# Kernel optimization log

Hardware: AMD Instinct MI355X
Metric: run time of the kernel (lower is better)

Reference implementation:

```python
import jax, jax.numpy as jnp
import numpy as np

N_WIN = 7
NUM_HEADS = 8
DIM = 256
QK = 256
TOPK = 4
MLP_HID = 4 * DIM
SCALE = QK ** -0.5  # used for both region routing and pixel attention (qk_scale=None)


def _layernorm(x, g, b, eps=1e-6):
    mu = jnp.mean(x, axis=-1, keepdims=True)
    var = jnp.mean(jnp.square(x - mu), axis=-1, keepdims=True)
    return (x - mu) * jax.lax.rsqrt(var + eps) * g + b


def _dwconv(x, w, b):
    # x: NHWC, w: (5,5,1,C) depthwise kernel (torch Conv2d groups=C, padding=2)
    y = jax.lax.conv_general_dilated(
        x, w, window_strides=(1, 1), padding='SAME',
        feature_group_count=x.shape[-1],
        dimension_numbers=('NHWC', 'HWIO', 'NHWC'))
    return y + b


def _bra(x, qkv_w, qkv_b, lepe_w, lepe_b, wo_w, wo_b):
    # BiLevelRoutingAttention, NHWC in/out
    N, H, W, C = x.shape
    j = i = N_WIN
    h, w = H // j, W // i
    p2, w2, m = j * i, h * w, NUM_HEADS
    dq, dv = QK // m, C // m
    # window partition: (N, p2, h, w, C)
    xw = x.reshape(N, j, h, i, w, C).transpose(0, 1, 3, 2, 4, 5).reshape(N, p2, h, w, C)
    qkv = xw @ qkv_w + qkv_b
    q = qkv[..., :QK]            # (N,p2,h,w,QK)
    kv = qkv[..., QK:]           # (N,p2,h,w,QK+C)
    q_pix = q.reshape(N, p2, w2, QK)
    kv_pix = kv.reshape(N, p2, w2, QK + C)
    q_win = jnp.mean(q, axis=(2, 3))                    # (N,p2,QK)
    k_win = jnp.mean(kv[..., :QK], axis=(2, 3))         # (N,p2,QK)
    # LePE: depthwise conv on V in full-image layout
    v_img = kv[..., QK:].reshape(N, j, i, h, w, C).transpose(0, 1, 3, 2, 4, 5).reshape(N, H, W, C)
    lepe = _dwconv(v_img, lepe_w, lepe_b)
    # region-to-region routing, top-k window selection
    logit = jnp.einsum('npc,nqc->npq', q_win * SCALE, k_win)    # (N,p2,p2)
    _, r_idx = jax.lax.top_k(logit, TOPK)                       # (N,p2,TOPK)
    # gather KV of selected windows: (N,p2,TOPK,w2,QK+C)
    kv_sel = kv_pix[jnp.arange(N)[:, None, None], r_idx]
    k_sel = kv_sel[..., :QK].reshape(N, p2, TOPK * w2, m, dq).transpose(0, 1, 3, 2, 4)  # (N,p2,m,kw2,dq)
    v_sel = kv_sel[..., QK:].reshape(N, p2, TOPK * w2, m, dv).transpose(0, 1, 3, 2, 4)  # (N,p2,m,kw2,dv)
    q_h = q_pix.reshape(N, p2, w2, m, dq).transpose(0, 1, 3, 2, 4)                      # (N,p2,m,w2,dq)
    aw = jnp.einsum('npmqd,npmkd->npmqk', q_h * SCALE, k_sel)
    aw = jax.nn.softmax(aw, axis=-1)
    out = jnp.einsum('npmqk,npmkd->npmqd', aw, v_sel)           # (N,p2,m,w2,dv)
    out = out.transpose(0, 1, 3, 2, 4).reshape(N, j, i, h, w, C)
    out = out.transpose(0, 1, 3, 2, 4, 5).reshape(N, H, W, C)
    out = out + lepe
    return out @ wo_w + wo_b


def setup_inputs() -> dict:
    key = jax.random.key(0)
    ks = jax.random.split(key, 8)
    s = 0.02
    return {
        'x': jax.random.normal(ks[0], (8, 56, 56, DIM), dtype=jnp.float32),
        'ln1_g': jnp.ones((DIM,), jnp.float32),
        'ln1_b': jnp.zeros((DIM,), jnp.float32),
        'qkv_w': jax.random.normal(ks[1], (DIM, 2 * QK + DIM), jnp.float32) * s,
        'qkv_b': jnp.zeros((2 * QK + DIM,), jnp.float32),
        'lepe_w': jax.random.normal(ks[2], (5, 5, 1, DIM), jnp.float32) * s,
        'lepe_b': jnp.zeros((DIM,), jnp.float32),
        'wo_w': jax.random.normal(ks[3], (DIM, DIM), jnp.float32) * s,
        'wo_b': jnp.zeros((DIM,), jnp.float32),
        'ln2_g': jnp.ones((DIM,), jnp.float32),
        'ln2_b': jnp.zeros((DIM,), jnp.float32),
        'mlp_w1': jax.random.normal(ks[4], (DIM, MLP_HID), jnp.float32) * s,
        'mlp_b1': jnp.zeros((MLP_HID,), jnp.float32),
        'mlp_w2': jax.random.normal(ks[5], (MLP_HID, DIM), jnp.float32) * s,
        'mlp_b2': jnp.zeros((DIM,), jnp.float32),
    }


def reference(x, ln1_g, ln1_b, qkv_w, qkv_b, lepe_w, lepe_b, wo_w, wo_b,
              ln2_g, ln2_b, mlp_w1, mlp_b1, mlp_w2, mlp_b2):
    x = x + _bra(_layernorm(x, ln1_g, ln1_b), qkv_w, qkv_b, lepe_w, lepe_b, wo_w, wo_b)
    h = _layernorm(x, ln2_g, ln2_b)
    h = jax.nn.gelu(h @ mlp_w1 + mlp_b1, approximate=False) @ mlp_w2 + mlp_b2
    return x + h
```

## Files before the change

### kernel.cpp

```cpp
#include <hip/hip_runtime.h>
#include <hip/hip_bf16.h>

#define NIMG 8
#define HW 56
#define CDIM 256
#define TOK (NIMG*HW*HW)
#define NWIN 49
#define NPW (NIMG*NWIN)
#define ATT_SCALE 0.0625f

typedef __attribute__((ext_vector_type(8))) short short8;
typedef __attribute__((ext_vector_type(4))) short short4v;
typedef __attribute__((ext_vector_type(4))) float f32x4;

static const size_t OFF_WQKV  = 0;
static const size_t OFF_WWO   = 393216;
static const size_t OFF_W1    = 524288;
static const size_t OFF_W2    = 1048576;
static const size_t OFF_XLN   = 1572864;
static const size_t OFF_QKV   = 14417920;
static const size_t OFF_QKWIN = 52953088;
static const size_t OFF_RIDX  = 53755904;
static const size_t OFF_ATTN  = 53762176;
static const size_t OFF_HMID  = OFF_XLN;

__device__ __forceinline__ float gelu_exact(float v) {
    return 0.5f * v * (1.f + erff(v * 0.70710678118654752f));
}
__device__ __forceinline__ short f2bs(float x) {
    __hip_bfloat16 h = __float2bfloat16(x);
    return *(short*)&h;
}
__device__ __forceinline__ float bs2f(short s) {
    return __uint_as_float(((unsigned)(unsigned short)s) << 16);
}
__device__ __forceinline__ void gld16(const short* g, short* l) {
    __builtin_amdgcn_global_load_lds(
        (const __attribute__((address_space(1))) void*)g,
        (__attribute__((address_space(3))) void*)l, 16, 0, 0);
}

__global__ __launch_bounds__(256) void transpose_cast4_k(const float* __restrict__ s0,
                                                         const float* __restrict__ s1,
                                                         const float* __restrict__ s2,
                                                         const float* __restrict__ s3,
                                                         __hip_bfloat16* __restrict__ d0,
                                                         __hip_bfloat16* __restrict__ d1,
                                                         __hip_bfloat16* __restrict__ d2,
                                                         __hip_bfloat16* __restrict__ d3) {
    int b = blockIdx.x;
    const float* src; __hip_bfloat16* dst; int K, N, l;
    if (b < 192)      { src = s0; dst = d0; K = 256;  N = 768;  l = b; }
    else if (b < 256) { src = s1; dst = d1; K = 256;  N = 256;  l = b - 192; }
    else if (b < 512) { src = s2; dst = d2; K = 256;  N = 1024; l = b - 256; }
    else              { src = s3; dst = d3; K = 1024; N = 256;  l = b - 512; }
    int nx = N / 32;
    int n0 = (l % nx) * 32, k0 = (l / nx) * 32;
    __shared__ float t[32][33];
    int tx = threadIdx.x & 31, ty = threadIdx.x >> 5;
    #pragma unroll
    for (int i = 0; i < 32; i += 8)
        t[ty + i][tx] = src[(size_t)(k0 + ty + i) * N + n0 + tx];
    __syncthreads();
    #pragma unroll
    for (int i = 0; i < 32; i += 8)
        dst[(size_t)(n0 + ty + i) * K + k0 + tx] = __float2bfloat16(t[tx][ty + i]);
}

__global__ __launch_bounds__(256) void ln_bf_k(const float* __restrict__ in,
                                               const float* __restrict__ g,
                                               const float* __restrict__ b,
                                               short* __restrict__ out, int remap) {
    int t = blockIdx.x * 4 + (threadIdx.x >> 6);
    int lane = threadIdx.x & 63;
    float4 v = *(const float4*)(in + (size_t)t * 256 + lane * 4);
    float s = v.x + v.y + v.z + v.w;
    float s2 = v.x * v.x + v.y * v.y + v.z * v.z + v.w * v.w;
    #pragma unroll
    for (int o = 32; o > 0; o >>= 1) {
        s  += __shfl_xor(s, o);
        s2 += __shfl_xor(s2, o);
    }
    float mu = s * (1.f / 256.f);
    float rstd = rsqrtf(s2 * (1.f / 256.f) - mu * mu + 1e-6f);
    float4 gv = *(const float4*)(g + lane * 4);
    float4 bv = *(const float4*)(b + lane * 4);
    short4v o;
    o[0] = f2bs((v.x - mu) * rstd * gv.x + bv.x);
    o[1] = f2bs((v.y - mu) * rstd * gv.y + bv.y);
    o[2] = f2bs((v.z - mu) * rstd * gv.z + bv.z);
    o[3] = f2bs((v.w - mu) * rstd * gv.w + bv.w);
    size_t tb;
    if (remap) {
        int n = t / 3136, rem = t % 3136, y = rem / 56, x = rem % 56;
        int p = (y >> 3) * 7 + (x >> 3);
        int si = (y & 7) * 8 + (x & 7);
        tb = (size_t)(n * 49 + p) * 64 + si;
    } else {
        tb = (size_t)t;
    }
    *(short4v*)(out + tb * 256 + lane * 4) = o;
}

__device__ __forceinline__ void mfma_step(const short* As, const short* Bs,
                                          int wm, int wn, int l15, int swr,
                                          f32x4 acc[2][4]) {
    short8 af[2], bfr[4];
    #pragma unroll
    for (int i = 0; i < 2; ++i)
        af[i] = *(const short8*)&As[(wm + i * 16 + l15) * 32 + swr];
    #pragma unroll
    for (int j = 0; j < 4; ++j)
        bfr[j] = *(const short8*)&Bs[(wn + j * 16 + l15) * 32 + swr];
    #pragma unroll
    for (int i = 0; i < 2; ++i)
        #pragma unroll
        for (int j = 0; j < 4; ++j)
            acc[i][j] = __builtin_amdgcn_mfma_f32_16x16x32_bf16(af[i], bfr[j], acc[i][j], 0, 0, 0);
}

template<int MODE>
__global__ __launch_bounds__(256) void gemm64(const short* __restrict__ A,
                                              const short* __restrict__ Bt,
                                              const float* __restrict__ bias,
                                              const float* __restrict__ res,
                                              void* Cv, float* __restrict__ winptr,
                                              int M, int N, int K) {
    const int bn = blockIdx.x * 128;
    const int bm = blockIdx.y * 64;
    const int tid = threadIdx.x;
    const int wave = tid >> 6, lane = tid & 63;
    const int l15 = lane & 15, quad = lane >> 4;
    const int wm = (wave & 1) * 32, wn = (wave >> 1) * 64;

    __shared__ __align__(16) short smem[18432];

    f32x4 acc[2][4];
    #pragma unroll
    for (int i = 0; i < 2; ++i)
        #pragma unroll
        for (int j = 0; j < 4; ++j) acc[i][j] = (f32x4){0.f, 0.f, 0.f, 0.f};

    const int srow = lane >> 2;
    const int scg  = ((lane & 3) ^ ((lane >> 3) & 3)) * 8;
    const short* ga  = A  + (size_t)(bm + wave * 16 + srow) * K + scg;
    const short* gb0 = Bt + (size_t)(bn + wave * 16 + srow) * K + scg;
    const short* gb1 = gb0 + (size_t)64 * K;
    const int swr = (quad ^ ((l15 >> 1) & 3)) * 8;

    const int nt = K >> 5;

    {
        short* b0 = smem;
        gld16(ga,       b0 + wave * 512);
        gld16(gb0,      b0 + 2048 + wave * 512);
        gld16(gb1,      b0 + 4096 + wave * 512);
        short* b1 = smem + 6144;
        gld16(ga  + 32, b1 + wave * 512);
        gld16(gb0 + 32, b1 + 2048 + wave * 512);
        gld16(gb1 + 32, b1 + 4096 + wave * 512);
    }

    for (int t = 0; t < nt; ++t) {
        if (t == nt - 1) asm volatile("s_waitcnt vmcnt(0)" ::: "memory");
        else             asm volatile("s_waitcnt vmcnt(3)" ::: "memory");
        __builtin_amdgcn_s_barrier();
        asm volatile("" ::: "memory");
        if (t + 2 < nt) {
            short* b = smem + ((t + 2) % 3) * 6144;
            int kk = (t + 2) * 32;
            gld16(ga  + kk, b + wave * 512);
            gld16(gb0 + kk, b + 2048 + wave * 512);
            gld16(gb1 + kk, b + 4096 + wave * 512);
        }
        const short* As = smem + (t % 3) * 6144;
        mfma_step(As, As + 2048, wm, wn, l15, swr, acc);
    }

    if (MODE == 0) {
        if (bn < 512) {
            float* wmean = (float*)&smem[12288];
            #pragma unroll
            for (int j = 0; j < 4; ++j) {
                float s = 0.f;
                #pragma unroll
                for (int i = 0; i < 2; ++i)
                    #pragma unroll
                    for (int r = 0; r < 4; ++r) s += acc[i][j][r];
                s += __shfl_xor(s, 16);
                s += __shfl_xor(s, 32);
                if (quad == 0) wmean[wave * 64 + j * 16 + l15] = s;
            }
            __syncthreads();
            if (tid < 128) {
                int c = tid;
                float s = (c < 64) ? (wmean[c] + wmean[64 + c])
                                   : (wmean[64 + c] + wmean[128 + c]);
                int col = bn + c;
                if (col < 512)
                    winptr[(size_t)blockIdx.y * 512 + col] = s * (1.f / 64.f) + bias[col];
            }
        }
    }

    if (MODE == 1) {
        #pragma unroll
        for (int i = 0; i < 2; ++i) {
            int row = bm + wm + i * 16 + quad * 4;
            #pragma unroll
            for (int j = 0; j < 4; ++j) {
                int col = bn + wn + j * 16 + l15;
                float bia = bias[col];
                #pragma unroll
                for (int r = 0; r < 4; ++r) {
                    size_t idx = (size_t)(row + r) * N + col;
                    ((float*)Cv)[idx] = acc[i][j][r] + bia + res[idx];
                }
            }
        }
    } else {
        asm volatile("s_waitcnt lgkmcnt(0)" ::: "memory");
        __builtin_amdgcn_s_barrier();
        asm volatile("" ::: "memory");
        float biasv[4];
        #pragma unroll
        for (int j = 0; j < 4; ++j) biasv[j] = bias[bn + wn + j * 16 + l15];
        short* ep = &smem[wave * 1280];
        short* outp = (short*)Cv;
        #pragma unroll
        for (int p = 0; p < 2; ++p) {
            #pragma unroll
            for (int i = 0; i < 2; ++i)
                #pragma unroll
                for (int jj = 0; jj < 2; ++jj) {
                    int j = p * 2 + jj;
                    #pragma unroll
                    for (int r = 0; r < 4; ++r) {
                        float v = acc[i][j][r] + biasv[j];
                        if (MODE == 2) v = gelu_exact(v);
                        ep[(i * 16 + quad * 4 + r) * 40 + jj * 16 + l15] = f2bs(v);
                    }
                }
            __builtin_amdgcn_s_waitcnt(0);
            int c = lane & 3;
            #pragma unroll
            for (int rr = 0; rr < 2; ++rr) {
                int row = rr * 16 + (lane >> 2);
                short8 v = *(const short8*)&ep[row * 40 + c * 8];
                *(short8*)&outp[(size_t)(bm + wm + row) * N + bn + wn + p * 32 + c * 8] = v;
            }
            __builtin_amdgcn_s_waitcnt(0);
        }
    }
}

__global__ __launch_bounds__(64) void route_k(const float* __restrict__ qkwin,
                                              int* __restrict__ ridx) {
    int w = blockIdx.x;
    int n = w / 49;
    int tid = threadIdx.x;
    __shared__ float qv[256];
    __shared__ float lg[49];
    for (int i = tid; i < 256; i += 64) qv[i] = qkwin[(size_t)w * 512 + i] * ATT_SCALE;
    __syncthreads();
    if (tid < 49) {
        const float* kp = qkwin + (size_t)(n * 49 + tid) * 512 + 256;
        float d = 0.f;
        for (int cc = 0; cc < 256; ++cc) d += qv[cc] * kp[cc];
        lg[tid] = d;
    }
    __syncthreads();
    if (tid == 0) {
        #pragma unroll
        for (int t = 0; t < 4; ++t) {
            float best = -1e30f; int bi = 0;
            for (int j = 0; j < 49; ++j)
                if (lg[j] > best) { best = lg[j]; bi = j; }
            lg[bi] = -1e30f;
            ridx[w * 4 + t] = bi;
        }
    }
}

__global__ __launch_bounds__(256) void attn_mfma_k(const short* __restrict__ qkv,
                                                   const int* __restrict__ ridx,
                                                   short* __restrict__ attn) {
    const int blk = blockIdx.x;
    const int w = blk >> 3, h = blk & 7;
    const int n = w / 49;
    const int tid = threadIdx.x;
    const int wave = tid >> 6, lane = tid & 63;
    const int l15 = lane & 15, quad = lane >> 4;

    __shared__ __align__(16) short smem[25344];
    short* Vt = smem;
    short* Ks = smem + 8448;
    short* Ps = smem + 8448;
    __shared__ int rs4[4];
    if (tid < 4) rs4[tid] = ridx[w * 4 + tid];
    __syncthreads();

    {
        int s = tid >> 2, kq = (tid & 3) * 8;
        #pragma unroll
        for (int u = 0; u < 4; ++u) {
            int key = u * 64 + s;
            const short* src = qkv + ((size_t)(n * 49 + rs4[u]) * 64 + s) * 768 + 256 + h * 32 + kq;
            *(short8*)&Ks[key * 40 + kq] = *(const short8*)src;
        }
    }
    {
        int kp = tid & 127, dh = tid >> 7;
        int k0 = kp * 2;
        int t = k0 >> 6, s = k0 & 63;
        const short* src0 = qkv + ((size_t)(n * 49 + rs4[t]) * 64 + s) * 768 + 512 + h * 32 + dh * 16;
        const short* src1 = src0 + 768;
        short8 a0 = *(const short8*)src0, a1 = *(const short8*)(src0 + 8);
        short8 b0 = *(const short8*)src1, b1 = *(const short8*)(src1 + 8);
        #pragma unroll
        for (int d = 0; d < 8; ++d) {
            *(unsigned*)&Vt[(dh * 16 + d) * 264 + k0] =
                (unsigned)(unsigned short)a0[d] | ((unsigned)(unsigned short)b0[d] << 16);
            *(unsigned*)&Vt[(dh * 16 + 8 + d) * 264 + k0] =
                (unsigned)(unsigned short)a1[d] | ((unsigned)(unsigned short)b1[d] << 16);
        }
    }
    __syncthreads();

    const short* qp = qkv + ((size_t)w * 64 + wave * 16 + l15) * 768 + h * 32 + quad * 8;
    short8 qf = *(const short8*)qp;

    f32x4 st[16];
    #pragma unroll
    for (int j = 0; j < 16; ++j) {
        short8 kf = *(const short8*)&Ks[(j * 16 + l15) * 40 + quad * 8];
        st[j] = __builtin_amdgcn_mfma_f32_16x16x32_bf16(kf, qf, (f32x4){0.f, 0.f, 0.f, 0.f}, 0, 0, 0);
    }

    float mx = -1e30f;
    #pragma unroll
    for (int j = 0; j < 16; ++j)
        #pragma unroll
        for (int r = 0; r < 4; ++r) mx = fmaxf(mx, st[j][r]);
    mx = fmaxf(mx, __shfl_xor(mx, 16));
    mx = fmaxf(mx, __shfl_xor(mx, 32));

    __syncthreads();

    short* pw = &Ps[wave * 16 * 264];
    float sum = 0.f;
    #pragma unroll
    for (int j = 0; j < 16; ++j) {
        short4v pv;
        #pragma unroll
        for (int r = 0; r < 4; ++r) {
            float p = __expf((st[j][r] - mx) * ATT_SCALE);
            sum += p;
            pv[r] = f2bs(p);
        }
        *(short4v*)&pw[l15 * 264 + j * 16 + quad * 4] = pv;
    }
    sum += __shfl_xor(sum, 16);
    sum += __shfl_xor(sum, 32);
    float inv = 1.f / sum;
    __builtin_amdgcn_s_waitcnt(0);

    f32x4 oc[2] = {(f32x4){0.f,0.f,0.f,0.f}, (f32x4){0.f,0.f,0.f,0.f}};
    #pragma unroll
    for (int kk = 0; kk < 8; ++kk) {
        short8 pf = *(const short8*)&pw[l15 * 264 + kk * 32 + quad * 8];
        #pragma unroll
        for (int jj = 0; jj < 2; ++jj) {
            short8 vf = *(const short8*)&Vt[(jj * 16 + l15) * 264 + kk * 32 + quad * 8];
            oc[jj] = __builtin_amdgcn_mfma_f32_16x16x32_bf16(vf, pf, oc[jj], 0, 0, 0);
        }
    }

    short* op = attn + ((size_t)w * 64 + wave * 16 + l15) * 256 + h * 32;
    #pragma unroll
    for (int jj = 0; jj < 2; ++jj) {
        short4v o4;
        #pragma unroll
        for (int r = 0; r < 4; ++r) o4[r] = f2bs(oc[jj][r] * inv);
        *(short4v*)&op[jj * 16 + quad * 4] = o4;
    }
}

__global__ __launch_bounds__(256) void lepe_k(const short* __restrict__ qkv,
                                              const short* __restrict__ attn,
                                              const float* __restrict__ lw,
                                              const float* __restrict__ lb,
                                              short* __restrict__ ywo) {
    int t = blockIdx.x * 8 + (threadIdx.x >> 5);
    int c0 = (threadIdx.x & 31) * 8;
    int n = t / 3136, rem = t % 3136, y = rem / 56, x = rem % 56;
    float sum[8];
    {
        float4 b0 = *(const float4*)(lb + c0), b1 = *(const float4*)(lb + c0 + 4);
        sum[0] = b0.x; sum[1] = b0.y; sum[2] = b0.z; sum[3] = b0.w;
        sum[4] = b1.x; sum[5] = b1.y; sum[6] = b1.z; sum[7] = b1.w;
    }
    #pragma unroll
    for (int ky = 0; ky < 5; ++ky) {
        int yy = y + ky - 2;
        if ((unsigned)yy >= 56u) continue;
        #pragma unroll
        for (int kx = 0; kx < 5; ++kx) {
            int xx = x + kx - 2;
            if ((unsigned)xx >= 56u) continue;
            int p = (yy >> 3) * 7 + (xx >> 3);
            int si = (yy & 7) * 8 + (xx & 7);
            short8 v = *(const short8*)(qkv + ((size_t)(n * 49 + p) * 64 + si) * 768 + 512 + c0);
            const float* wp = lw + (ky * 5 + kx) * 256 + c0;
            float4 w0 = *(const float4*)wp, w1 = *(const float4*)(wp + 4);
            sum[0] += bs2f(v[0]) * w0.x; sum[1] += bs2f(v[1]) * w0.y;
            sum[2] += bs2f(v[2]) * w0.z; sum[3] += bs2f(v[3]) * w0.w;
            sum[4] += bs2f(v[4]) * w1.x; sum[5] += bs2f(v[5]) * w1.y;
            sum[6] += bs2f(v[6]) * w1.z; sum[7] += bs2f(v[7]) * w1.w;
        }
    }
    int p0 = (y >> 3) * 7 + (x >> 3);
    int s0 = (y & 7) * 8 + (x & 7);
    short8 a = *(const short8*)(attn + ((size_t)(n * 49 + p0) * 64 + s0) * 256 + c0);
    short8 o;
    #pragma unroll
    for (int i = 0; i < 8; ++i) o[i] = f2bs(sum[i] + bs2f(a[i]));
    *(short8*)(ywo + (size_t)t * 256 + c0) = o;
}

extern "C" void kernel_launch(void* const* d_in, const int* in_sizes, int n_in,
                              void* d_out, int out_size, void* d_ws, size_t ws_size,
                              hipStream_t stream) {
    const float* x      = (const float*)d_in[0];
    const float* ln1_g  = (const float*)d_in[1];
    const float* ln1_b  = (const float*)d_in[2];
    const float* qkv_w  = (const float*)d_in[3];
    const float* qkv_b  = (const float*)d_in[4];
    const float* lepe_w = (const float*)d_in[5];
    const float* lepe_b = (const float*)d_in[6];
    const float* wo_w   = (const float*)d_in[7];
    const float* wo_b   = (const float*)d_in[8];
    const float* ln2_g  = (const float*)d_in[9];
    const float* ln2_b  = (const float*)d_in[10];
    const float* mlp_w1 = (const float*)d_in[11];
    const float* mlp_b1 = (const float*)d_in[12];
    const float* mlp_w2 = (const float*)d_in[13];
    const float* mlp_b2 = (const float*)d_in[14];
    float* out = (float*)d_out;

    char* ws = (char*)d_ws;
    __hip_bfloat16* wqkvT = (__hip_bfloat16*)(ws + OFF_WQKV);
    __hip_bfloat16* wwoT  = (__hip_bfloat16*)(ws + OFF_WWO);
    __hip_bfloat16* w1T   = (__hip_bfloat16*)(ws + OFF_W1);
    __hip_bfloat16* w2T   = (__hip_bfloat16*)(ws + OFF_W2);
    short* xln   = (short*)(ws + OFF_XLN);
    short* qkvb  = (short*)(ws + OFF_QKV);
    float* qkwin = (float*)(ws + OFF_QKWIN);
    int*   ridx  = (int*)(ws + OFF_RIDX);
    short* attnb = (short*)(ws + OFF_ATTN);
    short* ywo   = (short*)(ws + OFF_XLN);
    short* h2    = (short*)(ws + OFF_ATTN);
    short* hmid  = (short*)(ws + OFF_HMID);

    transpose_cast4_k<<<768, 256, 0, stream>>>(qkv_w, wo_w, mlp_w1, mlp_w2,
                                               wqkvT, wwoT, w1T, w2T);
    ln_bf_k<<<TOK/4, 256, 0, stream>>>(x, ln1_g, ln1_b, xln, 1);
    gemm64<0><<<dim3(6, 392), 256, 0, stream>>>(xln, (const short*)wqkvT,
                                                qkv_b, nullptr, qkvb, qkwin, TOK, 768, 256);
    route_k<<<NPW, 64, 0, stream>>>(qkwin, ridx);
    attn_mfma_k<<<NPW * 8, 256, 0, stream>>>(qkvb, ridx, attnb);
    lepe_k<<<TOK/8, 256, 0, stream>>>(qkvb, attnb, lepe_w, lepe_b, ywo);
    gemm64<1><<<dim3(2, 392), 256, 0, stream>>>(ywo, (const short*)wwoT,
                                                wo_b, x, out, nullptr, TOK, 256, 256);
    ln_bf_k<<<TOK/4, 256, 0, stream>>>(out, ln2_g, ln2_b, h2, 0);
    gemm64<2><<<dim3(8, 392), 256, 0, stream>>>(h2, (const short*)w1T,
                                                mlp_b1, nullptr, hmid, nullptr, TOK, 1024, 256);
    gemm64<1><<<dim3(2, 392), 256, 0, stream>>>(hmid, (const short*)w2T,
                                                mlp_b2, out, out, nullptr, TOK, 256, 1024);
}
```

Baseline: 293.6 us.

## Fuse output projection GEMM with residual add and second LayerNorm

Replaces the Wo GEMM plus separate LayerNorm kernel with one kernel in which each block computes a full 64x256 row tile. The kernel adds bias and residual, writes the fp32 output, then reduces row sums across waves in shared memory and writes the bf16 normalized activations. This removes one launch and a full re-read of the fp32 output for LayerNorm. In exchange it uses a 64-row tile over all 256 columns with fewer blocks (392), and computes variance in one pass as E[x^2]-mu^2.

```diff
diff --git a/kernel.cpp b/kernel.cpp
--- a/kernel.cpp
+++ b/kernel.cpp
@@ -250,6 +250,143 @@
                 *(short8*)&outp[(size_t)(bm + wm + row) * N + bn + wn + p * 32 + c * 8] = v;
             }
             __builtin_amdgcn_s_waitcnt(0);
+        }
+    }
+}
+
+__global__ __launch_bounds__(256) void gemm_woln_k(const short* __restrict__ A,
+                                                   const short* __restrict__ Bt,
+                                                   const float* __restrict__ bias,
+                                                   const float* __restrict__ res,
+                                                   const float* __restrict__ g2,
+                                                   const float* __restrict__ b2,
+                                                   float* __restrict__ out,
+                                                   short* __restrict__ h2) {
+    const int K = 256;
+    const int bm = blockIdx.x * 64;
+    const int tid = threadIdx.x;
+    const int wave = tid >> 6, lane = tid & 63;
+    const int l15 = lane & 15, quad = lane >> 4;
+    const int wn = wave * 64;
+
+    __shared__ __align__(16) short smem[30720];
+
+    f32x4 acc[4][4];
+    #pragma unroll
+    for (int i = 0; i < 4; ++i)
+        #pragma unroll
+        for (int j = 0; j < 4; ++j) acc[i][j] = (f32x4){0.f, 0.f, 0.f, 0.f};
+
+    const int srow = lane >> 2;
+    const int scg  = ((lane & 3) ^ ((lane >> 3) & 3)) * 8;
+    const short* ga  = A  + (size_t)(bm + wave * 16 + srow) * K + scg;
+    const short* gb  = Bt + (size_t)(wn + srow) * K + scg;
+    const int swr = (quad ^ ((l15 >> 1) & 3)) * 8;
+
+    const int nt = 8;
+
+    #define WOLN_STAGE(T) do {                                              \
+        short* _b = smem + ((T) % 3) * 10240;                               \
+        int _kk = (T) * 32;                                                 \
+        gld16(ga + _kk, _b + wave * 512);                                   \
+        _Pragma("unroll")                                                   \
+        for (int X = 0; X < 4; ++X)                                         \
+            gld16(gb + (size_t)X * 16 * K + _kk,                            \
+                  _b + 2048 + (wave * 4 + X) * 512);                        \
+    } while (0)
+
+    WOLN_STAGE(0);
+    WOLN_STAGE(1);
+
+    for (int t = 0; t < nt; ++t) {
+        if (t == nt - 1) asm volatile("s_waitcnt vmcnt(0)" ::: "memory");
+        else             asm volatile("s_waitcnt vmcnt(5)" ::: "memory");
+        __builtin_amdgcn_s_barrier();
+        asm volatile("" ::: "memory");
+        if (t + 2 < nt) WOLN_STAGE(t + 2);
+        const short* As = smem + (t % 3) * 10240;
+        const short* Bs = As + 2048;
+        short8 af[4], bfr[4];
+        #pragma unroll
+        for (int i = 0; i < 4; ++i)
+            af[i] = *(const short8*)&As[(i * 16 + l15) * 32 + swr];
+        #pragma unroll
+        for (int j = 0; j < 4; ++j)
+            bfr[j] = *(const short8*)&Bs[(wn + j * 16 + l15) * 32 + swr];
+        #pragma unroll
+        for (int i = 0; i < 4; ++i)
+            #pragma unroll
+            for (int j = 0; j < 4; ++j)
+                acc[i][j] = __builtin_amdgcn_mfma_f32_16x16x32_bf16(af[i], bfr[j], acc[i][j], 0, 0, 0);
+    }
+    #undef WOLN_STAGE
+
+    float bv4[4];
+    #pragma unroll
+    for (int j = 0; j < 4; ++j) bv4[j] = bias[wn + j * 16 + l15];
+    #pragma unroll
+    for (int i = 0; i < 4; ++i) {
+        int row = bm + i * 16 + quad * 4;
+        #pragma unroll
+        for (int j = 0; j < 4; ++j) {
+            int col = wn + j * 16 + l15;
+            #pragma unroll
+            for (int r = 0; r < 4; ++r) {
+                size_t idx = (size_t)(row + r) * 256 + col;
+                float y = acc[i][j][r] + bv4[j] + res[idx];
+                out[idx] = y;
+                acc[i][j][r] = y;
+            }
+        }
+    }
+
+    float* S1 = (float*)smem;
+    float* S2 = (float*)smem + 256;
+    #pragma unroll
+    for (int i = 0; i < 4; ++i) {
+        #pragma unroll
+        for (int r = 0; r < 4; ++r) {
+            float s1 = 0.f, s2 = 0.f;
+            #pragma unroll
+            for (int j = 0; j < 4; ++j) {
+                float y = acc[i][j][r];
+                s1 += y; s2 += y * y;
+            }
+            #pragma unroll
+            for (int o = 1; o < 16; o <<= 1) {
+                s1 += __shfl_xor(s1, o);
+                s2 += __shfl_xor(s2, o);
+            }
+            if (l15 == 0) {
+                int R = i * 16 + quad * 4 + r;
+                S1[wave * 64 + R] = s1;
+                S2[wave * 64 + R] = s2;
+            }
+        }
+    }
+    __syncthreads();
+
+    float gv4[4], bb4[4];
+    #pragma unroll
+    for (int j = 0; j < 4; ++j) {
+        gv4[j] = g2[wn + j * 16 + l15];
+        bb4[j] = b2[wn + j * 16 + l15];
+    }
+    #pragma unroll
+    for (int i = 0; i < 4; ++i) {
+        #pragma unroll
+        for (int r = 0; r < 4; ++r) {
+            int R = i * 16 + quad * 4 + r;
+            float t1 = S1[R] + S1[64 + R] + S1[128 + R] + S1[192 + R];
+            float t2 = S2[R] + S2[64 + R] + S2[128 + R] + S2[192 + R];
+            float mu = t1 * (1.f / 256.f);
+            float rstd = rsqrtf(t2 * (1.f / 256.f) - mu * mu + 1e-6f);
+            #pragma unroll
+            for (int j = 0; j < 4; ++j) {
+                int col = wn + j * 16 + l15;
+                h2[(size_t)(bm + R) * 256 + col] =
+                    f2bs((acc[i][j][r] - mu) * rstd * gv4[j] + bb4[j]);
+            }
         }
     }
 }
@@ -470,9 +607,8 @@
     route_k<<<NPW, 64, 0, stream>>>(qkwin, ridx);
     attn_mfma_k<<<NPW * 8, 256, 0, stream>>>(qkvb, ridx, attnb);
     lepe_k<<<TOK/8, 256, 0, stream>>>(qkvb, attnb, lepe_w, lepe_b, ywo);
-    gemm64<1><<<dim3(2, 392), 256, 0, stream>>>(ywo, (const short*)wwoT,
-                                                wo_b, x, out, nullptr, TOK, 256, 256);
-    ln_bf_k<<<TOK/4, 256, 0, stream>>>(out, ln2_g, ln2_b, h2, 0);
+    gemm_woln_k<<<TOK/64, 256, 0, stream>>>(ywo, (const short*)wwoT, wo_b, x,
+                                            ln2_g, ln2_b, out, h2);
     gemm64<2><<<dim3(8, 392), 256, 0, stream>>>(h2, (const short*)w1T,
                                                 mlp_b1, nullptr, hmid, nullptr, TOK, 1024, 256);
     gemm64<1><<<dim3(2, 392), 256, 0, stream>>>(hmid, (const short*)w2T,
```

Result: faster. 285.3 us (-2.8%).
